# Optimization experiments

Hardware: AMD Instinct MI355X
Metric: run time of the kernel (lower is better)

The kernel has to match this reference:

```python
import jax, jax.numpy as jnp
import numpy as np

B, N, DIM = 32, 577, 768   # N = num_patches + 1
H, DH = 12, 64             # heads, dim_head; inner_dim = H*DH = 768
NEG = -987654321.0         # LSA diagonal mask value from the source


def setup_inputs() -> dict:
    key = jax.random.key(0)
    ks = jax.random.split(key, 5)
    inner = H * DH
    base_scale = DH ** -0.5
    return {
        "x": jax.random.normal(ks[0], (B, N, DIM), dtype=jnp.float32),
        "W_qkv": jax.random.normal(ks[1], (DIM, inner * 3), dtype=jnp.float32) * (DIM ** -0.5),
        "scale": base_scale * (1.0 + 0.01 * jax.random.normal(ks[2], (H,), dtype=jnp.float32)),
        "W_out": jax.random.normal(ks[3], (inner, DIM), dtype=jnp.float32) * (inner ** -0.5),
        "b_out": jnp.zeros((DIM,), dtype=jnp.float32),
    }


def reference(x, W_qkv, scale, W_out, b_out):
    b, n, _ = x.shape
    qkv = x @ W_qkv                                   # [b, n, 3*H*DH]
    q, k, v = jnp.split(qkv, 3, axis=-1)
    to_heads = lambda t: t.reshape(b, n, H, DH).transpose(0, 2, 1, 3)  # b h n d
    q, k, v = to_heads(q), to_heads(k), to_heads(v)
    # per-head learnable scale (LSA)
    dots = jnp.einsum('bhid,bhjd->bhij', q, k) * scale[None, :, None, None]
    # mask self-attention diagonal (eye scatter in the torch source)
    eye = jnp.eye(n, dtype=bool)
    dots = jnp.where(eye[None, None], NEG, dots)
    attn = jax.nn.softmax(dots, axis=-1)
    out = jnp.einsum('bhij,bhjd->bhid', attn, v)      # b h n d
    out = out.transpose(0, 2, 1, 3).reshape(b, n, H * DH)
    return out @ W_out + b_out
```

## Files before the change

### kernel.cpp

```cpp
#include <hip/hip_runtime.h>


typedef _Float16 half8  __attribute__((ext_vector_type(8)));
typedef _Float16 h4f    __attribute__((ext_vector_type(4)));
typedef __fp16   hv2    __attribute__((ext_vector_type(2)));
typedef __fp16   hv4    __attribute__((ext_vector_type(4)));
typedef float    floatx4 __attribute__((ext_vector_type(4)));

#define MTOT   18464
#define NEG_V  (-987654321.0f)
#define VTS    584

__device__ __forceinline__ void gl_lds16(const _Float16* g, _Float16* l) {
    __builtin_amdgcn_global_load_lds(
        (const __attribute__((address_space(1))) unsigned int*)g,
        (__attribute__((address_space(3))) unsigned int*)l,
        16, 0, 0);
}

__global__ __launch_bounds__(256) void cvt_x(const float* __restrict__ x,
                                             _Float16* __restrict__ x16) {
    const size_t idx = ((size_t)blockIdx.x * 256 + threadIdx.x) * 8;
    half8 h = {};
    if (idx < (size_t)MTOT * 768) {
        float4 a = *(const float4*)(x + idx);
        float4 b = *(const float4*)(x + idx + 4);
        h[0] = (_Float16)a.x; h[1] = (_Float16)a.y;
        h[2] = (_Float16)a.z; h[3] = (_Float16)a.w;
        h[4] = (_Float16)b.x; h[5] = (_Float16)b.y;
        h[6] = (_Float16)b.z; h[7] = (_Float16)b.w;
    }
    *(half8*)(x16 + idx) = h;
}

__global__ __launch_bounds__(256) void transpose_w(const float* __restrict__ src,
                                                   _Float16* __restrict__ dst,
                                                   int K, int Ncol) {
    __shared__ float tile[32][33];
    const int n0 = blockIdx.x * 32, k0 = blockIdx.y * 32;
    const int tx = threadIdx.x & 31, ty = threadIdx.x >> 5;
    for (int i = 0; i < 32; i += 8)
        tile[ty + i][tx] = src[(size_t)(k0 + ty + i) * Ncol + (n0 + tx)];
    __syncthreads();
    for (int i = 0; i < 32; i += 8)
        dst[(size_t)(n0 + ty + i) * K + (k0 + tx)] = (_Float16)tile[tx][ty + i];
}

__global__ __launch_bounds__(256, 4) void gemm_qkv(const _Float16* __restrict__ x16,
                                                   const _Float16* __restrict__ wT,
                                                   const float* __restrict__ scale,
                                                   _Float16* __restrict__ qg,
                                                   _Float16* __restrict__ kg,
                                                   _Float16* __restrict__ vT) {
    __shared__ _Float16 As[2][128 * 32];
    __shared__ _Float16 Bs[2][128 * 32];
    const unsigned orig = blockIdx.x;
    const unsigned xcd = orig & 7u, bidx = orig >> 3;
    const unsigned swz = (xcd < 2u ? xcd * 327u : 654u + (xcd - 2u) * 326u) + bidx;
    const unsigned mi = swz / 18u, ni = swz - mi * 18u;
    const int m0 = (int)mi * 128, n0 = (int)ni * 128;
    const int tid = threadIdx.x;
    const int lane = tid & 63, wv = tid >> 6;
    const int wrow = wv >> 1, wcol = wv & 1;
    const int lr = lane & 15, lq = lane >> 4;

    const int r1 = tid >> 2,        c1 = (((tid & 3) ^ ((r1 >> 1) & 3)) * 8);
    const int r2 = 64 + (tid >> 2), c2 = (((tid & 3) ^ ((r2 >> 1) & 3)) * 8);
    const int xc = (lq ^ ((lr >> 1) & 3)) * 8;

    floatx4 acc[4][4];
    const floatx4 fz = {0.f, 0.f, 0.f, 0.f};
    for (int i = 0; i < 4; ++i)
        for (int j = 0; j < 4; ++j) acc[i][j] = fz;

    #define STAGE_QKV(ki, bfx)                                                      \
        do {                                                                        \
            const int kk_ = (ki) * 32;                                              \
            gl_lds16(x16 + (size_t)(m0 + r1) * 768 + kk_ + c1, &As[bfx][wv*64*8]);  \
            gl_lds16(x16 + (size_t)(m0 + r2) * 768 + kk_ + c2,                      \
                     &As[bfx][(256 + wv*64) * 8]);                                  \
            gl_lds16(wT + (size_t)(n0 + r1) * 768 + kk_ + c1, &Bs[bfx][wv*64*8]);   \
            gl_lds16(wT + (size_t)(n0 + r2) * 768 + kk_ + c2,                       \
                     &Bs[bfx][(256 + wv*64) * 8]);                                  \
        } while (0)

    STAGE_QKV(0, 0);
    for (int ki = 0; ki < 24; ++ki) {
        const int bf = ki & 1;
        if (ki < 23) {
            STAGE_QKV(ki + 1, bf ^ 1);
            asm volatile("s_waitcnt vmcnt(4)" ::: "memory");
        } else {
            asm volatile("s_waitcnt vmcnt(0)" ::: "memory");
        }
        asm volatile("s_barrier" ::: "memory");

        half8 af[4], bfr[4];
        #pragma unroll
        for (int i = 0; i < 4; ++i)
            af[i] = *(const half8*)&As[bf][(wrow * 64 + i * 16 + lr) * 32 + xc];
        #pragma unroll
        for (int j = 0; j < 4; ++j)
            bfr[j] = *(const half8*)&Bs[bf][(wcol * 64 + j * 16 + lr) * 32 + xc];
        #pragma unroll
        for (int i = 0; i < 4; ++i)
            #pragma unroll
            for (int j = 0; j < 4; ++j)
                acc[i][j] = __builtin_amdgcn_mfma_f32_16x16x32_f16(af[i], bfr[j], acc[i][j], 0, 0, 0);

        asm volatile("s_waitcnt lgkmcnt(0)\n\ts_barrier" ::: "memory");
    }
    #undef STAGE_QKV

    const int cbase = n0 + wcol * 64;
    const int which = cbase / 768;
    const int h = (cbase - which * 768) >> 6;
    const float qsc = (which == 0) ? scale[h] * 1.4426950408889634f : 1.0f;
    #pragma unroll
    for (int j = 0; j < 4; ++j) {
        const int d = j * 16 + lr;
        #pragma unroll
        for (int i = 0; i < 4; ++i)
            #pragma unroll
            for (int r = 0; r < 4; ++r) {
                const int row = m0 + wrow * 64 + i * 16 + lq * 4 + r;
                if (row >= MTOT) continue;
                const unsigned bb = (unsigned)row / 577u;
                const unsigned nn = (unsigned)row - bb * 577u;
                const _Float16 val = (_Float16)(acc[i][j][r] * qsc);
                const size_t head = (size_t)(bb * 12 + h);
                if (which == 0)      qg[(head * 577 + nn) * 64 + d] = val;
                else if (which == 1) kg[(head * 577 + nn) * 64 + d] = val;
                else                 vT[(head * 64 + d) * VTS + nn] = val;
            }
    }
}

__global__ __launch_bounds__(256) void attn_kernel(const _Float16* __restrict__ qg,
                                                   const _Float16* __restrict__ kg,
                                                   const _Float16* __restrict__ vT,
                                                   _Float16* __restrict__ Og) {
    __shared__ __align__(16) _Float16 Ks[2][64 * 64];
    __shared__ __align__(16) _Float16 Vs[2][64 * 64];
    const unsigned orig = blockIdx.x;
    const unsigned swz = (orig & 7u) * 240u + (orig >> 3);
    const int qt = (int)(swz % 5u);
    const unsigned hb = swz / 5u;
    const int h = (int)(hb % 12u), b = (int)(hb / 12u);
    const int tid = threadIdx.x, lane = tid & 63, wv = tid >> 6;
    const int lr = lane & 15, lq = lane >> 4;
    const size_t head = (size_t)(b * 12 + h);
    const _Float16* qh = qg + head * 577 * 64;
    const _Float16* kh = kg + head * 577 * 64;
    const _Float16* vh = vT + head * 64 * VTS;
    const int q0 = qt * 128;
    const int xs = lq ^ (lr & 7), xs4 = xs ^ 4;

    half8 bq[2][2];
    #pragma unroll
    for (int st = 0; st < 2; ++st) {
        const int qi = q0 + st * 64 + wv * 16 + lr;
        const int qc = qi < 577 ? qi : 576;
        bq[st][0] = *(const half8*)(qh + (size_t)qc * 64 + lq * 8);
        bq[st][1] = *(const half8*)(qh + (size_t)qc * 64 + 32 + lq * 8);
    }

    #define PREF(kt_, pb_)                                               \
        do {                                                             \
            const int j0_ = (kt_) * 64;                                  \
            {   const int c_ = wv * 64 + lane;                           \
                const int r_ = c_ >> 3, cl_ = (c_ & 7) ^ (r_ & 7);       \
                gl_lds16(kh + (size_t)(j0_ + r_) * 64 + cl_ * 8,         \
                         &Ks[pb_][(wv * 64) * 8]);                       \
                gl_lds16(vh + (size_t)r_ * VTS + j0_ + cl_ * 8,          \
                         &Vs[pb_][(wv * 64) * 8]);   }                   \
            {   const int c_ = 256 + wv * 64 + lane;                     \
                const int r_ = c_ >> 3, cl_ = (c_ & 7) ^ (r_ & 7);       \
                gl_lds16(kh + (size_t)(j0_ + r_) * 64 + cl_ * 8,         \
                         &Ks[pb_][(256 + wv * 64) * 8]);                 \
                gl_lds16(vh + (size_t)r_ * VTS + j0_ + cl_ * 8,          \
                         &Vs[pb_][(256 + wv * 64) * 8]);   }             \
        } while (0)

    const floatx4 fz = {0.f, 0.f, 0.f, 0.f};
    floatx4 ot[2][4];
    #pragma unroll
    for (int st = 0; st < 2; ++st)
        #pragma unroll
        for (int c = 0; c < 4; ++c) ot[st][c] = fz;
    float sacc[2] = {0.f, 0.f};

    PREF(0, 0);
    for (int kt = 0; kt < 10; ++kt) {
        const int bf = kt & 1;
        if (kt < 9) {
            PREF(kt + 1, bf ^ 1);
            asm volatile("s_waitcnt vmcnt(4)" ::: "memory");
        } else {
            asm volatile("s_waitcnt vmcnt(0)" ::: "memory");
        }
        asm volatile("s_barrier" ::: "memory");

        half8 ak[4][2];
        #pragma unroll
        for (int ct = 0; ct < 4; ++ct) {
            const int base = (ct * 16 + lr) * 64;
            ak[ct][0] = *(const half8*)&Ks[bf][base + xs * 8];
            ak[ct][1] = *(const half8*)&Ks[bf][base + xs4 * 8];
        }

        floatx4 s[2][4];
        #pragma unroll
        for (int st = 0; st < 2; ++st)
            #pragma unroll
            for (int ct = 0; ct < 4; ++ct) {
                floatx4 t = __builtin_amdgcn_mfma_f32_16x16x32_f16(ak[ct][0], bq[st][0], fz, 0, 0, 0);
                s[st][ct] = __builtin_amdgcn_mfma_f32_16x16x32_f16(ak[ct][1], bq[st][1], t, 0, 0, 0);
            }

        if (kt == 9) {
            #pragma unroll
            for (int st = 0; st < 2; ++st) {
                s[st][0][0] = (lq == 0) ? s[st][0][0] : -INFINITY;
                s[st][0][1] = -INFINITY; s[st][0][2] = -INFINITY; s[st][0][3] = -INFINITY;
                #pragma unroll
                for (int ct = 1; ct < 4; ++ct) {
                    s[st][ct][0] = -INFINITY; s[st][ct][1] = -INFINITY;
                    s[st][ct][2] = -INFINITY; s[st][ct][3] = -INFINITY;
                }
            }
        }
        #pragma unroll
        for (int st = 0; st < 2; ++st) {
            if (kt == qt * 2 + st) {
                #pragma unroll
                for (int ct = 0; ct < 4; ++ct)
                    if (ct == wv) {
                        #pragma unroll
                        for (int r = 0; r < 4; ++r)
                            if (lq * 4 + r == lr) s[st][ct][r] = -INFINITY;
                    }
            }
        }

        hv4 pk[2][4];
        #pragma unroll
        for (int st = 0; st < 2; ++st)
            #pragma unroll
            for (int ct = 0; ct < 4; ++ct) {
                const float p0 = __builtin_amdgcn_exp2f(s[st][ct][0]);
                const float p1 = __builtin_amdgcn_exp2f(s[st][ct][1]);
                const float p2 = __builtin_amdgcn_exp2f(s[st][ct][2]);
                const float p3 = __builtin_amdgcn_exp2f(s[st][ct][3]);
                sacc[st] += (p0 + p1) + (p2 + p3);
                const hv2 lo = __builtin_amdgcn_cvt_pkrtz(p0, p1);
                const hv2 hi = __builtin_amdgcn_cvt_pkrtz(p2, p3);
                pk[st][ct] = __builtin_shufflevector(lo, hi, 0, 1, 2, 3);
            }

        #pragma unroll
        for (int jc = 0; jc < 4; ++jc) {
            const int csv = ((jc << 1) | (lq >> 1)) ^ (lr & 7);
            #pragma unroll
            for (int ctd = 0; ctd < 4; ++ctd) {
                const hv4 av = *(const hv4*)&Vs[bf][(ctd * 16 + lr) * 64 + csv * 8 + (lq & 1) * 4];
                #pragma unroll
                for (int st = 0; st < 2; ++st)
                    ot[st][ctd] = __builtin_amdgcn_mfma_f32_16x16x16f16(av, pk[st][jc], ot[st][ctd], 0, 0, 0);
            }
        }

        asm volatile("s_waitcnt lgkmcnt(0)\n\ts_barrier" ::: "memory");
    }
    #undef PREF

    #pragma unroll
    for (int st = 0; st < 2; ++st) {
        float l = sacc[st];
        l += __shfl_xor(l, 16, 64);
        l += __shfl_xor(l, 32, 64);
        const float linv = 1.f / l;
        const int i = q0 + st * 64 + wv * 16 + lr;
        if (i < 577) {
            #pragma unroll
            for (int ctd = 0; ctd < 4; ++ctd) {
                h4f ov;
                #pragma unroll
                for (int r = 0; r < 4; ++r) ov[r] = (_Float16)(ot[st][ctd][r] * linv);
                *(h4f*)(Og + ((size_t)(b * 577 + i)) * 768 + h * 64 + ctd * 16 + lq * 4) = ov;
            }
        }
    }
}

__global__ __launch_bounds__(256, 4) void gemm_out(const _Float16* __restrict__ Og,
                                                   const _Float16* __restrict__ wT,
                                                   const float* __restrict__ bias,
                                                   float* __restrict__ out) {
    __shared__ _Float16 As[2][128 * 32];
    __shared__ _Float16 Bs[2][128 * 32];
    const unsigned orig = blockIdx.x;
    const unsigned xcd = orig & 7u, bidx = orig >> 3;
    const unsigned swz = (xcd < 6u ? xcd * 109u : 654u + (xcd - 6u) * 108u) + bidx;
    const unsigned mi = swz / 6u, ni = swz - mi * 6u;
    const int m0 = (int)mi * 128, n0 = (int)ni * 128;
    const int tid = threadIdx.x;
    const int lane = tid & 63, wv = tid >> 6;
    const int wrow = wv >> 1, wcol = wv & 1;
    const int lr = lane & 15, lq = lane >> 4;

    const int r1 = tid >> 2,        c1 = (((tid & 3) ^ ((r1 >> 1) & 3)) * 8);
    const int r2 = 64 + (tid >> 2), c2 = (((tid & 3) ^ ((r2 >> 1) & 3)) * 8);
    const int xc = (lq ^ ((lr >> 1) & 3)) * 8;

    floatx4 acc[4][4];
    const floatx4 fz = {0.f, 0.f, 0.f, 0.f};
    for (int i = 0; i < 4; ++i)
        for (int j = 0; j < 4; ++j) acc[i][j] = fz;

    #define STAGE_OUT(ki, bfx)                                                      \
        do {                                                                        \
            const int kk_ = (ki) * 32;                                              \
            gl_lds16(Og + (size_t)(m0 + r1) * 768 + kk_ + c1, &As[bfx][wv*64*8]);   \
            gl_lds16(Og + (size_t)(m0 + r2) * 768 + kk_ + c2,                       \
                     &As[bfx][(256 + wv*64) * 8]);                                  \
            gl_lds16(wT + (size_t)(n0 + r1) * 768 + kk_ + c1, &Bs[bfx][wv*64*8]);   \
            gl_lds16(wT + (size_t)(n0 + r2) * 768 + kk_ + c2,                       \
                     &Bs[bfx][(256 + wv*64) * 8]);                                  \
        } while (0)

    STAGE_OUT(0, 0);
    for (int ki = 0; ki < 24; ++ki) {
        const int bf = ki & 1;
        if (ki < 23) {
            STAGE_OUT(ki + 1, bf ^ 1);
            asm volatile("s_waitcnt vmcnt(4)" ::: "memory");
        } else {
            asm volatile("s_waitcnt vmcnt(0)" ::: "memory");
        }
        asm volatile("s_barrier" ::: "memory");

        half8 af[4], bfr[4];
        #pragma unroll
        for (int i = 0; i < 4; ++i)
            af[i] = *(const half8*)&As[bf][(wrow * 64 + i * 16 + lr) * 32 + xc];
        #pragma unroll
        for (int j = 0; j < 4; ++j)
            bfr[j] = *(const half8*)&Bs[bf][(wcol * 64 + j * 16 + lr) * 32 + xc];
        #pragma unroll
        for (int i = 0; i < 4; ++i)
            #pragma unroll
            for (int j = 0; j < 4; ++j)
                acc[i][j] = __builtin_amdgcn_mfma_f32_16x16x32_f16(af[i], bfr[j], acc[i][j], 0, 0, 0);

        asm volatile("s_waitcnt lgkmcnt(0)\n\ts_barrier" ::: "memory");
    }
    #undef STAGE_OUT

    #pragma unroll
    for (int j = 0; j < 4; ++j) {
        const int c = n0 + wcol * 64 + j * 16 + lr;
        const float bv = bias[c];
        #pragma unroll
        for (int i = 0; i < 4; ++i)
            #pragma unroll
            for (int r = 0; r < 4; ++r) {
                const int row = m0 + wrow * 64 + i * 16 + lq * 4 + r;
                if (row < MTOT) out[(size_t)row * 768 + c] = acc[i][j][r] + bv;
            }
    }
}

extern "C" void kernel_launch(void* const* d_in, const int* in_sizes, int n_in,
                              void* d_out, int out_size, void* d_ws, size_t ws_size,
                              hipStream_t stream) {
    const float* x      = (const float*)d_in[0];
    const float* W_qkv  = (const float*)d_in[1];
    const float* scale  = (const float*)d_in[2];
    const float* W_out  = (const float*)d_in[3];
    const float* b_out  = (const float*)d_in[4];
    float* out = (float*)d_out;

    char* ws = (char*)d_ws;
    _Float16* x16   = (_Float16*)(ws);
    _Float16* Og    = x16;
    _Float16* qg    = (_Float16*)(ws + 28508160u);
    _Float16* kg    = (_Float16*)(ws + 28508160u + 28360704u);
    _Float16* vT    = (_Float16*)(ws + 28508160u + 2u * 28360704u);
    _Float16* WqkvT = (_Float16*)(ws + 28508160u + 2u * 28360704u + 28704768u);
    _Float16* WoutT = WqkvT + (size_t)2304 * 768;

    cvt_x<<<6960, 256, 0, stream>>>(x, x16);
    transpose_w<<<dim3(72, 24), 256, 0, stream>>>(W_qkv, WqkvT, 768, 2304);
    transpose_w<<<dim3(24, 24), 256, 0, stream>>>(W_out, WoutT, 768, 768);
    gemm_qkv<<<2610, 256, 0, stream>>>(x16, WqkvT, scale, qg, kg, vT);
    attn_kernel<<<1920, 256, 0, stream>>>(qg, kg, vT, Og);
    gemm_out<<<870, 256, 0, stream>>>(Og, WoutT, b_out, out);
}
```

Measured before the change: 346.3 us.

## Widen GEMM tiles to 128x256 with 8 waves and K=64 split-phase pipeline

Both projection GEMMs now use 512-thread blocks computing 128x256 output tiles with a K step of 64. Each K step is split into two halves, and the next tile's global-to-LDS loads are interleaved between them. s_setprio is raised around the MFMA bursts, and the LDS swizzle is changed to an 8-way XOR. The larger tile improves operand reuse and halves the number of barriers per K, at the cost of fewer blocks (occupancy of 2 blocks per CU) and a larger LDS footprint.

```diff
diff --git a/kernel.cpp b/kernel.cpp
--- a/kernel.cpp
+++ b/kernel.cpp
@@ -46,71 +46,99 @@
         dst[(size_t)(n0 + ty + i) * K + (k0 + tx)] = (_Float16)tile[tx][ty + i];
 }
 
-__global__ __launch_bounds__(256, 4) void gemm_qkv(const _Float16* __restrict__ x16,
+__global__ __launch_bounds__(512, 2) void gemm_qkv(const _Float16* __restrict__ x16,
                                                    const _Float16* __restrict__ wT,
                                                    const float* __restrict__ scale,
                                                    _Float16* __restrict__ qg,
                                                    _Float16* __restrict__ kg,
                                                    _Float16* __restrict__ vT) {
-    __shared__ _Float16 As[2][128 * 32];
-    __shared__ _Float16 Bs[2][128 * 32];
+    __shared__ _Float16 As[2][128 * 64];
+    __shared__ _Float16 Bs[2][256 * 64];
     const unsigned orig = blockIdx.x;
     const unsigned xcd = orig & 7u, bidx = orig >> 3;
-    const unsigned swz = (xcd < 2u ? xcd * 327u : 654u + (xcd - 2u) * 326u) + bidx;
-    const unsigned mi = swz / 18u, ni = swz - mi * 18u;
-    const int m0 = (int)mi * 128, n0 = (int)ni * 128;
+    const unsigned swz = (xcd == 0u ? 0u : 164u + (xcd - 1u) * 163u) + bidx;
+    const unsigned mi = swz / 9u, ni = swz - mi * 9u;
+    const int m0 = (int)mi * 128, n0 = (int)ni * 256;
     const int tid = threadIdx.x;
     const int lane = tid & 63, wv = tid >> 6;
-    const int wrow = wv >> 1, wcol = wv & 1;
+    const int wrow = wv >> 2, wcol = wv & 3;
     const int lr = lane & 15, lq = lane >> 4;
 
-    const int r1 = tid >> 2,        c1 = (((tid & 3) ^ ((r1 >> 1) & 3)) * 8);
-    const int r2 = 64 + (tid >> 2), c2 = (((tid & 3) ^ ((r2 >> 1) & 3)) * 8);
-    const int xc = (lq ^ ((lr >> 1) & 3)) * 8;
+    const int rA  = tid >> 3;
+    const int cl8 = ((tid & 7) ^ (rA & 7)) * 8;
+    const int x0 = (lq ^ (lr & 7)) * 8;
+    const int x1 = ((4 + lq) ^ (lr & 7)) * 8;
 
     floatx4 acc[4][4];
     const floatx4 fz = {0.f, 0.f, 0.f, 0.f};
     for (int i = 0; i < 4; ++i)
         for (int j = 0; j < 4; ++j) acc[i][j] = fz;
 
-    #define STAGE_QKV(ki, bfx)                                                      \
+    #define ST_P0(ki, bfx)                                                          \
         do {                                                                        \
-            const int kk_ = (ki) * 32;                                              \
-            gl_lds16(x16 + (size_t)(m0 + r1) * 768 + kk_ + c1, &As[bfx][wv*64*8]);  \
-            gl_lds16(x16 + (size_t)(m0 + r2) * 768 + kk_ + c2,                      \
-                     &As[bfx][(256 + wv*64) * 8]);                                  \
-            gl_lds16(wT + (size_t)(n0 + r1) * 768 + kk_ + c1, &Bs[bfx][wv*64*8]);   \
-            gl_lds16(wT + (size_t)(n0 + r2) * 768 + kk_ + c2,                       \
-                     &Bs[bfx][(256 + wv*64) * 8]);                                  \
+            const int kk_ = (ki) * 64;                                              \
+            gl_lds16(x16 + (size_t)(m0 + rA) * 768 + kk_ + cl8,                     \
+                     &As[bfx][(wv * 64) * 8]);                                      \
+            gl_lds16(wT + (size_t)(n0 + rA) * 768 + kk_ + cl8,                      \
+                     &Bs[bfx][(wv * 64) * 8]);                                      \
+            gl_lds16(wT + (size_t)(n0 + 64 + rA) * 768 + kk_ + cl8,                 \
+                     &Bs[bfx][(512 + wv * 64) * 8]);                                \
         } while (0)
-
-    STAGE_QKV(0, 0);
-    for (int ki = 0; ki < 24; ++ki) {
-        const int bf = ki & 1;
-        if (ki < 23) {
-            STAGE_QKV(ki + 1, bf ^ 1);
-            asm volatile("s_waitcnt vmcnt(4)" ::: "memory");
-        } else {
-            asm volatile("s_waitcnt vmcnt(0)" ::: "memory");
-        }
-        asm volatile("s_barrier" ::: "memory");
-
+    #define ST_P1(ki, bfx)                                                          \
+        do {                                                                        \
+            const int kk_ = (ki) * 64;                                              \
+            gl_lds16(x16 + (size_t)(m0 + 64 + rA) * 768 + kk_ + cl8,                \
+                     &As[bfx][(512 + wv * 64) * 8]);                                \
+            gl_lds16(wT + (size_t)(n0 + 128 + rA) * 768 + kk_ + cl8,                \
+                     &Bs[bfx][(1024 + wv * 64) * 8]);                               \
+            gl_lds16(wT + (size_t)(n0 + 192 + rA) * 768 + kk_ + cl8,                \
+                     &Bs[bfx][(1536 + wv * 64) * 8]);                               \
+        } while (0)
+
+    ST_P0(0, 0); ST_P1(0, 0);
+    asm volatile("s_waitcnt vmcnt(0)" ::: "memory");
+    asm volatile("s_barrier" ::: "memory");
+
+    for (int kt = 0; kt < 12; ++kt) {
+        const int bf = kt & 1;
         half8 af[4], bfr[4];
         #pragma unroll
         for (int i = 0; i < 4; ++i)
-            af[i] = *(const half8*)&As[bf][(wrow * 64 + i * 16 + lr) * 32 + xc];
+            af[i] = *(const half8*)&As[bf][(wrow * 64 + i * 16 + lr) * 64 + x0];
         #pragma unroll
         for (int j = 0; j < 4; ++j)
-            bfr[j] = *(const half8*)&Bs[bf][(wcol * 64 + j * 16 + lr) * 32 + xc];
+            bfr[j] = *(const half8*)&Bs[bf][(wcol * 64 + j * 16 + lr) * 64 + x0];
+        if (kt < 11) ST_P0(kt + 1, bf ^ 1);
+        asm volatile("s_barrier" ::: "memory");
+        __builtin_amdgcn_s_setprio(1);
         #pragma unroll
         for (int i = 0; i < 4; ++i)
             #pragma unroll
             for (int j = 0; j < 4; ++j)
                 acc[i][j] = __builtin_amdgcn_mfma_f32_16x16x32_f16(af[i], bfr[j], acc[i][j], 0, 0, 0);
-
-        asm volatile("s_waitcnt lgkmcnt(0)\n\ts_barrier" ::: "memory");
-    }
-    #undef STAGE_QKV
+        __builtin_amdgcn_s_setprio(0);
+        asm volatile("s_barrier" ::: "memory");
+
+        #pragma unroll
+        for (int i = 0; i < 4; ++i)
+            af[i] = *(const half8*)&As[bf][(wrow * 64 + i * 16 + lr) * 64 + x1];
+        #pragma unroll
+        for (int j = 0; j < 4; ++j)
+            bfr[j] = *(const half8*)&Bs[bf][(wcol * 64 + j * 16 + lr) * 64 + x1];
+        if (kt < 11) ST_P1(kt + 1, bf ^ 1);
+        asm volatile("s_barrier" ::: "memory");
+        __builtin_amdgcn_s_setprio(1);
+        #pragma unroll
+        for (int i = 0; i < 4; ++i)
+            #pragma unroll
+            for (int j = 0; j < 4; ++j)
+                acc[i][j] = __builtin_amdgcn_mfma_f32_16x16x32_f16(af[i], bfr[j], acc[i][j], 0, 0, 0);
+        __builtin_amdgcn_s_setprio(0);
+        if (kt < 11) asm volatile("s_waitcnt vmcnt(0)" ::: "memory");
+        asm volatile("s_barrier" ::: "memory");
+    }
+    #undef ST_P0
+    #undef ST_P1
 
     const int cbase = n0 + wcol * 64;
     const int which = cbase / 768;
@@ -293,69 +321,97 @@
     }
 }
 
-__global__ __launch_bounds__(256, 4) void gemm_out(const _Float16* __restrict__ Og,
+__global__ __launch_bounds__(512, 2) void gemm_out(const _Float16* __restrict__ Og,
                                                    const _Float16* __restrict__ wT,
                                                    const float* __restrict__ bias,
                                                    float* __restrict__ out) {
-    __shared__ _Float16 As[2][128 * 32];
-    __shared__ _Float16 Bs[2][128 * 32];
+    __shared__ _Float16 As[2][128 * 64];
+    __shared__ _Float16 Bs[2][256 * 64];
     const unsigned orig = blockIdx.x;
     const unsigned xcd = orig & 7u, bidx = orig >> 3;
-    const unsigned swz = (xcd < 6u ? xcd * 109u : 654u + (xcd - 6u) * 108u) + bidx;
-    const unsigned mi = swz / 6u, ni = swz - mi * 6u;
-    const int m0 = (int)mi * 128, n0 = (int)ni * 128;
+    const unsigned swz = (xcd < 3u ? xcd * 55u : 165u + (xcd - 3u) * 54u) + bidx;
+    const unsigned mi = swz / 3u, ni = swz - mi * 3u;
+    const int m0 = (int)mi * 128, n0 = (int)ni * 256;
     const int tid = threadIdx.x;
     const int lane = tid & 63, wv = tid >> 6;
-    const int wrow = wv >> 1, wcol = wv & 1;
+    const int wrow = wv >> 2, wcol = wv & 3;
     const int lr = lane & 15, lq = lane >> 4;
 
-    const int r1 = tid >> 2,        c1 = (((tid & 3) ^ ((r1 >> 1) & 3)) * 8);
-    const int r2 = 64 + (tid >> 2), c2 = (((tid & 3) ^ ((r2 >> 1) & 3)) * 8);
-    const int xc = (lq ^ ((lr >> 1) & 3)) * 8;
+    const int rA  = tid >> 3;
+    const int cl8 = ((tid & 7) ^ (rA & 7)) * 8;
+    const int x0 = (lq ^ (lr & 7)) * 8;
+    const int x1 = ((4 + lq) ^ (lr & 7)) * 8;
 
     floatx4 acc[4][4];
     const floatx4 fz = {0.f, 0.f, 0.f, 0.f};
     for (int i = 0; i < 4; ++i)
         for (int j = 0; j < 4; ++j) acc[i][j] = fz;
 
-    #define STAGE_OUT(ki, bfx)                                                      \
+    #define ST_P0(ki, bfx)                                                          \
         do {                                                                        \
-            const int kk_ = (ki) * 32;                                              \
-            gl_lds16(Og + (size_t)(m0 + r1) * 768 + kk_ + c1, &As[bfx][wv*64*8]);   \
-            gl_lds16(Og + (size_t)(m0 + r2) * 768 + kk_ + c2,                       \
-                     &As[bfx][(256 + wv*64) * 8]);                                  \
-            gl_lds16(wT + (size_t)(n0 + r1) * 768 + kk_ + c1, &Bs[bfx][wv*64*8]);   \
-            gl_lds16(wT + (size_t)(n0 + r2) * 768 + kk_ + c2,                       \
-                     &Bs[bfx][(256 + wv*64) * 8]);                                  \
+            const int kk_ = (ki) * 64;                                              \
+            gl_lds16(Og + (size_t)(m0 + rA) * 768 + kk_ + cl8,                      \
+                     &As[bfx][(wv * 64) * 8]);                                      \
+            gl_lds16(wT + (size_t)(n0 + rA) * 768 + kk_ + cl8,                      \
+                     &Bs[bfx][(wv * 64) * 8]);                                      \
+            gl_lds16(wT + (size_t)(n0 + 64 + rA) * 768 + kk_ + cl8,                 \
+                     &Bs[bfx][(512 + wv * 64) * 8]);                                \
         } while (0)
-
-    STAGE_OUT(0, 0);
-    for (int ki = 0; ki < 24; ++ki) {
-        const int bf = ki & 1;
-        if (ki < 23) {
-            STAGE_OUT(ki + 1, bf ^ 1);
-            asm volatile("s_waitcnt vmcnt(4)" ::: "memory");
-        } else {
-            asm volatile("s_waitcnt vmcnt(0)" ::: "memory");
-        }
-        asm volatile("s_barrier" ::: "memory");
-
+    #define ST_P1(ki, bfx)                                                          \
+        do {                                                                        \
+            const int kk_ = (ki) * 64;                                              \
+            gl_lds16(Og + (size_t)(m0 + 64 + rA) * 768 + kk_ + cl8,                 \
+                     &As[bfx][(512 + wv * 64) * 8]);                                \
+            gl_lds16(wT + (size_t)(n0 + 128 + rA) * 768 + kk_ + cl8,                \
+                     &Bs[bfx][(1024 + wv * 64) * 8]);                               \
+            gl_lds16(wT + (size_t)(n0 + 192 + rA) * 768 + kk_ + cl8,                \
+                     &Bs[bfx][(1536 + wv * 64) * 8]);                               \
+        } while (0)
+
+    ST_P0(0, 0); ST_P1(0, 0);
+    asm volatile("s_waitcnt vmcnt(0)" ::: "memory");
+    asm volatile("s_barrier" ::: "memory");
+
+    for (int kt = 0; kt < 12; ++kt) {
+        const int bf = kt & 1;
         half8 af[4], bfr[4];
         #pragma unroll
         for (int i = 0; i < 4; ++i)
-            af[i] = *(const half8*)&As[bf][(wrow * 64 + i * 16 + lr) * 32 + xc];
+            af[i] = *(const half8*)&As[bf][(wrow * 64 + i * 16 + lr) * 64 + x0];
         #pragma unroll
         for (int j = 0; j < 4; ++j)
-            bfr[j] = *(const half8*)&Bs[bf][(wcol * 64 + j * 16 + lr) * 32 + xc];
+            bfr[j] = *(const half8*)&Bs[bf][(wcol * 64 + j * 16 + lr) * 64 + x0];
+        if (kt < 11) ST_P0(kt + 1, bf ^ 1);
+        asm volatile("s_barrier" ::: "memory");
+        __builtin_amdgcn_s_setprio(1);
         #pragma unroll
         for (int i = 0; i < 4; ++i)
             #pragma unroll
             for (int j = 0; j < 4; ++j)
                 acc[i][j] = __builtin_amdgcn_mfma_f32_16x16x32_f16(af[i], bfr[j], acc[i][j], 0, 0, 0);
-
-        asm volatile("s_waitcnt lgkmcnt(0)\n\ts_barrier" ::: "memory");
-    }
-    #undef STAGE_OUT
+        __builtin_amdgcn_s_setprio(0);
+        asm volatile("s_barrier" ::: "memory");
+
+        #pragma unroll
+        for (int i = 0; i < 4; ++i)
+            af[i] = *(const half8*)&As[bf][(wrow * 64 + i * 16 + lr) * 64 + x1];
+        #pragma unroll
+        for (int j = 0; j < 4; ++j)
+            bfr[j] = *(const half8*)&Bs[bf][(wcol * 64 + j * 16 + lr) * 64 + x1];
+        if (kt < 11) ST_P1(kt + 1, bf ^ 1);
+        asm volatile("s_barrier" ::: "memory");
+        __builtin_amdgcn_s_setprio(1);
+        #pragma unroll
+        for (int i = 0; i < 4; ++i)
+            #pragma unroll
+            for (int j = 0; j < 4; ++j)
+                acc[i][j] = __builtin_amdgcn_mfma_f32_16x16x32_f16(af[i], bfr[j], acc[i][j], 0, 0, 0);
+        __builtin_amdgcn_s_setprio(0);
+        if (kt < 11) asm volatile("s_waitcnt vmcnt(0)" ::: "memory");
+        asm volatile("s_barrier" ::: "memory");
+    }
+    #undef ST_P0
+    #undef ST_P1
 
     #pragma unroll
     for (int j = 0; j < 4; ++j) {
@@ -393,7 +449,7 @@
     cvt_x<<<6960, 256, 0, stream>>>(x, x16);
     transpose_w<<<dim3(72, 24), 256, 0, stream>>>(W_qkv, WqkvT, 768, 2304);
     transpose_w<<<dim3(24, 24), 256, 0, stream>>>(W_out, WoutT, 768, 768);
-    gemm_qkv<<<2610, 256, 0, stream>>>(x16, WqkvT, scale, qg, kg, vT);
+    gemm_qkv<<<1305, 512, 0, stream>>>(x16, WqkvT, scale, qg, kg, vT);
     attn_kernel<<<1920, 256, 0, stream>>>(qg, kg, vT, Og);
-    gemm_out<<<870, 256, 0, stream>>>(Og, WoutT, b_out, out);
-}
+    gemm_out<<<435, 512, 0, stream>>>(Og, WoutT, b_out, out);
+}
```

Measured after the change: 367.1 us. 1.06x slower.

## Fuse fp32-to-fp16 conversion of x into QKV GEMM A-tile loading

Applied to the files above, without the earlier changes.

Drops the separate cvt_x kernel. The QKV GEMM now loads fp32 x directly into registers, converts it to fp16 and writes the A tile to LDS, with the load software-pipelined one k-step ahead. It also merges the two weight-transpose launches into a single kernel. The aim is to remove a full extra pass over x and two launches, at the cost of larger fp32 global reads per GEMM tile (x is re-read by all 18 column tiles at twice the bytes) and more register pressure in the GEMM main loop.

```diff
diff --git a/kernel.cpp b/kernel.cpp
--- a/kernel.cpp
+++ b/kernel.cpp
@@ -18,35 +18,31 @@
         16, 0, 0);
 }
 
-__global__ __launch_bounds__(256) void cvt_x(const float* __restrict__ x,
-                                             _Float16* __restrict__ x16) {
-    const size_t idx = ((size_t)blockIdx.x * 256 + threadIdx.x) * 8;
-    half8 h = {};
-    if (idx < (size_t)MTOT * 768) {
-        float4 a = *(const float4*)(x + idx);
-        float4 b = *(const float4*)(x + idx + 4);
-        h[0] = (_Float16)a.x; h[1] = (_Float16)a.y;
-        h[2] = (_Float16)a.z; h[3] = (_Float16)a.w;
-        h[4] = (_Float16)b.x; h[5] = (_Float16)b.y;
-        h[6] = (_Float16)b.z; h[7] = (_Float16)b.w;
-    }
-    *(half8*)(x16 + idx) = h;
-}
-
-__global__ __launch_bounds__(256) void transpose_w(const float* __restrict__ src,
-                                                   _Float16* __restrict__ dst,
-                                                   int K, int Ncol) {
+__global__ __launch_bounds__(256) void transpose_both(const float* __restrict__ Wqkv,
+                                                      const float* __restrict__ Wout,
+                                                      _Float16* __restrict__ WqkvT,
+                                                      _Float16* __restrict__ WoutT) {
+    const float* src;
+    _Float16* dst;
+    int Ncol, k0, n0;
+    if (blockIdx.y < 24) {
+        src = Wqkv; dst = WqkvT; Ncol = 2304;
+        k0 = blockIdx.y * 32; n0 = blockIdx.x * 32;
+    } else {
+        if (blockIdx.x >= 24) return;
+        src = Wout; dst = WoutT; Ncol = 768;
+        k0 = (blockIdx.y - 24) * 32; n0 = blockIdx.x * 32;
+    }
     __shared__ float tile[32][33];
-    const int n0 = blockIdx.x * 32, k0 = blockIdx.y * 32;
     const int tx = threadIdx.x & 31, ty = threadIdx.x >> 5;
     for (int i = 0; i < 32; i += 8)
         tile[ty + i][tx] = src[(size_t)(k0 + ty + i) * Ncol + (n0 + tx)];
     __syncthreads();
     for (int i = 0; i < 32; i += 8)
-        dst[(size_t)(n0 + ty + i) * K + (k0 + tx)] = (_Float16)tile[tx][ty + i];
-}
-
-__global__ __launch_bounds__(256, 4) void gemm_qkv(const _Float16* __restrict__ x16,
+        dst[(size_t)(n0 + ty + i) * 768 + (k0 + tx)] = (_Float16)tile[tx][ty + i];
+}
+
+__global__ __launch_bounds__(256, 4) void gemm_qkv(const float* __restrict__ x,
                                                    const _Float16* __restrict__ wT,
                                                    const float* __restrict__ scale,
                                                    _Float16* __restrict__ qg,
@@ -68,30 +64,62 @@
     const int r2 = 64 + (tid >> 2), c2 = (((tid & 3) ^ ((r2 >> 1) & 3)) * 8);
     const int xc = (lq ^ ((lr >> 1) & 3)) * 8;
 
+    const int rr1 = (m0 + r1 < MTOT) ? (m0 + r1) : (MTOT - 1);
+    const int rr2 = (m0 + r2 < MTOT) ? (m0 + r2) : (MTOT - 1);
+    const float* xp1 = x + (size_t)rr1 * 768 + c1;
+    const float* xp2 = x + (size_t)rr2 * 768 + c2;
+    _Float16* wd1[2] = { &As[0][wv * 512 + lane * 8], &As[1][wv * 512 + lane * 8] };
+    _Float16* wd2[2] = { &As[0][2048 + wv * 512 + lane * 8], &As[1][2048 + wv * 512 + lane * 8] };
+
     floatx4 acc[4][4];
     const floatx4 fz = {0.f, 0.f, 0.f, 0.f};
     for (int i = 0; i < 4; ++i)
         for (int j = 0; j < 4; ++j) acc[i][j] = fz;
 
-    #define STAGE_QKV(ki, bfx)                                                      \
+    float4 la0, la1, la2, la3;
+    #define A_LOAD(ki)                                                              \
         do {                                                                        \
             const int kk_ = (ki) * 32;                                              \
-            gl_lds16(x16 + (size_t)(m0 + r1) * 768 + kk_ + c1, &As[bfx][wv*64*8]);  \
-            gl_lds16(x16 + (size_t)(m0 + r2) * 768 + kk_ + c2,                      \
-                     &As[bfx][(256 + wv*64) * 8]);                                  \
-            gl_lds16(wT + (size_t)(n0 + r1) * 768 + kk_ + c1, &Bs[bfx][wv*64*8]);   \
+            la0 = *(const float4*)(xp1 + kk_);                                      \
+            la1 = *(const float4*)(xp1 + kk_ + 4);                                  \
+            la2 = *(const float4*)(xp2 + kk_);                                      \
+            la3 = *(const float4*)(xp2 + kk_ + 4);                                  \
+        } while (0)
+    #define CVT_WRITE(B)                                                            \
+        do {                                                                        \
+            half8 h1, h2;                                                           \
+            h1[0] = (_Float16)la0.x; h1[1] = (_Float16)la0.y;                       \
+            h1[2] = (_Float16)la0.z; h1[3] = (_Float16)la0.w;                       \
+            h1[4] = (_Float16)la1.x; h1[5] = (_Float16)la1.y;                       \
+            h1[6] = (_Float16)la1.z; h1[7] = (_Float16)la1.w;                       \
+            h2[0] = (_Float16)la2.x; h2[1] = (_Float16)la2.y;                       \
+            h2[2] = (_Float16)la2.z; h2[3] = (_Float16)la2.w;                       \
+            h2[4] = (_Float16)la3.x; h2[5] = (_Float16)la3.y;                       \
+            h2[6] = (_Float16)la3.z; h2[7] = (_Float16)la3.w;                       \
+            *(half8*)wd1[B] = h1;                                                   \
+            *(half8*)wd2[B] = h2;                                                   \
+        } while (0)
+    #define B_STAGE(ki, B)                                                          \
+        do {                                                                        \
+            const int kk_ = (ki) * 32;                                              \
+            gl_lds16(wT + (size_t)(n0 + r1) * 768 + kk_ + c1, &Bs[B][wv*64*8]);     \
             gl_lds16(wT + (size_t)(n0 + r2) * 768 + kk_ + c2,                       \
-                     &Bs[bfx][(256 + wv*64) * 8]);                                  \
+                     &Bs[B][(256 + wv*64) * 8]);                                    \
         } while (0)
 
-    STAGE_QKV(0, 0);
+    A_LOAD(0);
+    B_STAGE(0, 0);
+    asm volatile("s_waitcnt vmcnt(2)" ::: "memory");
+    CVT_WRITE(0);
+
     for (int ki = 0; ki < 24; ++ki) {
         const int bf = ki & 1;
         if (ki < 23) {
-            STAGE_QKV(ki + 1, bf ^ 1);
-            asm volatile("s_waitcnt vmcnt(4)" ::: "memory");
+            A_LOAD(ki + 1);
+            B_STAGE(ki + 1, bf ^ 1);
+            asm volatile("s_waitcnt vmcnt(6) lgkmcnt(0)" ::: "memory");
         } else {
-            asm volatile("s_waitcnt vmcnt(0)" ::: "memory");
+            asm volatile("s_waitcnt vmcnt(0) lgkmcnt(0)" ::: "memory");
         }
         asm volatile("s_barrier" ::: "memory");
 
@@ -108,9 +136,15 @@
             for (int j = 0; j < 4; ++j)
                 acc[i][j] = __builtin_amdgcn_mfma_f32_16x16x32_f16(af[i], bfr[j], acc[i][j], 0, 0, 0);
 
+        if (ki < 23) {
+            asm volatile("s_waitcnt vmcnt(2)" ::: "memory");
+            CVT_WRITE(bf ^ 1);
+        }
         asm volatile("s_waitcnt lgkmcnt(0)\n\ts_barrier" ::: "memory");
     }
-    #undef STAGE_QKV
+    #undef A_LOAD
+    #undef CVT_WRITE
+    #undef B_STAGE
 
     const int cbase = n0 + wcol * 64;
     const int which = cbase / 768;
@@ -382,18 +416,15 @@
     float* out = (float*)d_out;
 
     char* ws = (char*)d_ws;
-    _Float16* x16   = (_Float16*)(ws);
-    _Float16* Og    = x16;
+    _Float16* Og    = (_Float16*)(ws);
     _Float16* qg    = (_Float16*)(ws + 28508160u);
     _Float16* kg    = (_Float16*)(ws + 28508160u + 28360704u);
     _Float16* vT    = (_Float16*)(ws + 28508160u + 2u * 28360704u);
     _Float16* WqkvT = (_Float16*)(ws + 28508160u + 2u * 28360704u + 28704768u);
     _Float16* WoutT = WqkvT + (size_t)2304 * 768;
 
-    cvt_x<<<6960, 256, 0, stream>>>(x, x16);
-    transpose_w<<<dim3(72, 24), 256, 0, stream>>>(W_qkv, WqkvT, 768, 2304);
-    transpose_w<<<dim3(24, 24), 256, 0, stream>>>(W_out, WoutT, 768, 768);
-    gemm_qkv<<<2610, 256, 0, stream>>>(x16, WqkvT, scale, qg, kg, vT);
+    transpose_both<<<dim3(72, 48), 256, 0, stream>>>(W_qkv, W_out, WqkvT, WoutT);
+    gemm_qkv<<<2610, 256, 0, stream>>>(x, WqkvT, scale, qg, kg, vT);
     attn_kernel<<<1920, 256, 0, stream>>>(qg, kg, vT, Og);
     gemm_out<<<870, 256, 0, stream>>>(Og, WoutT, b_out, out);
 }
```

Measured after the change: 439.8 us. 27.0% more time.
